# Kernel optimization log

Measured on AMD Instinct MI355X. Metric: run time of the kernel, lower is better.

## Reference

```python
import jax, jax.numpy as jnp
import numpy as np
from jax import lax

B, N, CIN, H, W = 1, 6, 256, 32, 88
COUT = 80
IMG_H, IMG_W = 256, 704
XB = (-51.2, 51.2, 0.8); YB = (-51.2, 51.2, 0.8); ZB = (-5.0, 3.0, 0.8)
NX, NY, NZ = 128, 128, 10
EPS = 1e-5


def _voxel_coords(b0, b1, vs):
    n = int(round((b1 - b0) / vs))
    return jnp.linspace(b0 + 0.5 * vs, b1 - 0.5 * vs, n, dtype=jnp.float32)


def _make_points():
    xs = _voxel_coords(*XB); ys = _voxel_coords(*YB); zs = _voxel_coords(*ZB)
    gx, gy, gz = jnp.meshgrid(xs, ys, zs, indexing='ij')
    return jnp.stack([gx, gy, gz], -1).reshape(-1, 3)  # [M,3], M = NX*NY*NZ


def _conv(x, w, b=None, pad=1):
    y = lax.conv_general_dilated(x, w, (1, 1), [(pad, pad), (pad, pad)],
                                 dimension_numbers=('NCHW', 'OIHW', 'NCHW'))
    if b is not None:
        y = y + b[None, :, None, None]
    return y


def _bn(x, g, b, m, v):
    return (g[None, :, None, None] * (x - m[None, :, None, None])
            * lax.rsqrt(v[None, :, None, None] + EPS) + b[None, :, None, None])


def _bilinear(feat, gx, gy):
    # feat [C,Hf,Wf]; gx,gy [M] in [-1,1]; align_corners=True, zero padding
    C, Hf, Wf = feat.shape
    ix = (gx + 1.0) * 0.5 * (Wf - 1)
    iy = (gy + 1.0) * 0.5 * (Hf - 1)
    ix0 = jnp.floor(ix); iy0 = jnp.floor(iy)
    wx1 = ix - ix0; wy1 = iy - iy0

    def tap(iyf, ixf, wgt):
        valid = (ixf >= 0) & (ixf < Wf) & (iyf >= 0) & (iyf < Hf)
        ii = jnp.clip(ixf, 0, Wf - 1).astype(jnp.int32)
        jj = jnp.clip(iyf, 0, Hf - 1).astype(jnp.int32)
        return feat[:, jj, ii] * (wgt * valid)[None, :]

    return (tap(iy0, ix0, (1 - wy1) * (1 - wx1))
            + tap(iy0, ix0 + 1, (1 - wy1) * wx1)
            + tap(iy0 + 1, ix0, wy1 * (1 - wx1))
            + tap(iy0 + 1, ix0 + 1, wy1 * wx1))


def reference(img, lidar2image, w1, b1, g1, beta1, m1, v1,
              w2, b2, g2, beta2, m2, v2, w3, b3):
    # proj_net: conv3x3+BN+ReLU, conv3x3+BN+ReLU, conv1x1
    x = img.reshape(B * N, CIN, H, W)
    x = jax.nn.relu(_bn(_conv(x, w1, b1), g1, beta1, m1, v1))
    x = jax.nn.relu(_bn(_conv(x, w2, b2), g2, beta2, m2, v2))
    feat = _conv(x, w3, b3, pad=0)  # [B*N, COUT, H, W]

    pts = _make_points()  # [M,3]
    R = lidar2image[:, :, :3, :3].reshape(B * N, 3, 3)
    t = lidar2image[:, :, :3, 3].reshape(B * N, 3, 1)
    proj = jnp.einsum('kij,mj->kim', R, pts) + t  # [BN,3,M]
    dist = proj[:, 2]
    px = proj[:, 0] / dist
    py = proj[:, 1] / dist
    gx = px / IMG_W * 2.0 - 1.0
    gy = py / IMG_H * 2.0 - 1.0

    sampled = jax.vmap(_bilinear)(feat, gx, gy)  # [BN, COUT, M]
    on_img = (px < IMG_W) & (px > 0) & (py < IMG_H) & (py > 0) & (dist > 0.1)
    sampled = jnp.where(on_img[:, None, :], sampled, 0.0)

    vox = sampled.reshape(B, N, COUT, NX, NY, NZ)
    bev = jnp.max(vox, axis=1).mean(axis=-1)  # [B, COUT, NX, NY]
    return bev


def setup_inputs() -> dict:
    key = jax.random.key(0)
    ks = jax.random.split(key, 8)
    img = jax.random.normal(ks[0], (B, N, CIN, H, W), jnp.float32)

    # Plausible lidar->image matrices: 6 cameras in a ring, pinhole intrinsics.
    fx = fy = 280.0; cx = IMG_W / 2.0; cy = IMG_H / 2.0
    K = np.array([[fx, 0.0, cx], [0.0, fy, cy], [0.0, 0.0, 1.0]])
    mats = []
    for k in range(N):
        th = 2.0 * np.pi * k / N
        fwd = np.array([np.cos(th), np.sin(th), 0.0])
        rgt = np.array([np.sin(th), -np.cos(th), 0.0])
        dwn = np.array([0.0, 0.0, -1.0])
        Rm = np.stack([rgt, dwn, fwd], 0)
        c = np.array([0.5 * np.cos(th), 0.5 * np.sin(th), 1.5])
        M4 = np.eye(4)
        M4[:3, :3] = K @ Rm
        M4[:3, 3] = K @ (-Rm @ c)
        mats.append(M4)
    lidar2image = jnp.asarray(np.broadcast_to(np.stack(mats), (B, N, 4, 4)).copy(),
                              jnp.float32)

    def w(k, shape, s=0.02):
        return jax.random.normal(k, shape, jnp.float32) * s

    zc = lambda c: jnp.zeros((c,), jnp.float32)
    oc = lambda c: jnp.ones((c,), jnp.float32)
    return dict(
        img=img, lidar2image=lidar2image,
        w1=w(ks[1], (CIN, CIN, 3, 3)), b1=zc(CIN),
        g1=oc(CIN), beta1=zc(CIN), m1=zc(CIN), v1=oc(CIN),
        w2=w(ks[2], (CIN, CIN, 3, 3)), b2=zc(CIN),
        g2=oc(CIN), beta2=zc(CIN), m2=zc(CIN), v2=oc(CIN),
        w3=w(ks[3], (COUT, CIN, 1, 1)), b3=zc(COUT),
    )
```

## Files before the change

### kernel.cpp

```cpp
#include <hip/hip_runtime.h>
#include <math.h>

#define N_IMG 6
#define CIN   256
#define H_IN  32
#define W_IN  88
#define SP    2816
#define COUTC 80
#define EPSBN 1e-5f

typedef _Float16 half8 __attribute__((ext_vector_type(8)));
typedef float floatx4 __attribute__((ext_vector_type(4)));

__global__ __launch_bounds__(256) void prep_w33(const float* __restrict__ w,
                                                _Float16* __restrict__ wT) {
  int idx = blockIdx.x * 256 + threadIdx.x;
  if (idx >= 9 * CIN * CIN) return;
  int oc  = idx / 2304;
  int r   = idx - oc * 2304;
  int tap = r >> 8;
  int ic  = r & 255;
  wT[idx] = (_Float16)w[(oc * CIN + ic) * 9 + tap];
}

__global__ __launch_bounds__(256) void prep_w11(const float* __restrict__ w,
                                                _Float16* __restrict__ wT) {
  int idx = blockIdx.x * 256 + threadIdx.x;
  if (idx >= CIN * COUTC) return;
  wT[idx] = (_Float16)w[idx];
}

__global__ __launch_bounds__(256) void nchw_to_nhwc(const float* __restrict__ img,
                                                    _Float16* __restrict__ x0) {
  __shared__ float t[64][65];
  const int sp0 = blockIdx.x * 64;
  const int ic0 = blockIdx.y * 64;
  const int im  = blockIdx.z;
  const int tx = threadIdx.x & 63;
  const int ty = threadIdx.x >> 6;
  for (int r = ty; r < 64; r += 4)
    t[r][tx] = img[((size_t)(im * CIN + ic0 + r)) * SP + sp0 + tx];
  __syncthreads();
  for (int r = ty; r < 64; r += 4)
    x0[((size_t)im * SP + sp0 + r) * CIN + ic0 + tx] = (_Float16)t[tx][r];
}

__global__ __launch_bounds__(256) void conv3x3_mfma(
    const _Float16* __restrict__ x, const _Float16* __restrict__ wT,
    const float* __restrict__ bias, const float* __restrict__ gamma,
    const float* __restrict__ beta, const float* __restrict__ bnm,
    const float* __restrict__ bnv, _Float16* __restrict__ out)
{
  __shared__ _Float16 As[128 * 72];
  __shared__ _Float16 Bs[128 * 72];

  const int tid = threadIdx.x;
  const int m0 = blockIdx.x * 128;
  const int n0 = blockIdx.y * 128;
  const int im = blockIdx.z;

  int rr[4], kk4[4], hh[4], ww[4];
  #pragma unroll
  for (int i = 0; i < 4; ++i) {
    const int c = tid + 256 * i;
    rr[i]  = c >> 3;
    kk4[i] = (c & 7) * 8;
    const int m = m0 + rr[i];
    hh[i] = m / 88;
    ww[i] = m - hh[i] * 88;
  }
  const _Float16* xim = x + (size_t)im * SP * CIN;

  const int lane = tid & 63;
  const int wv = tid >> 6;
  const int mw = (wv & 1) * 64;
  const int nw = (wv >> 1) * 64;
  const int fr = lane & 15;
  const int q8 = (lane >> 4) * 8;
  const int q4 = (lane >> 4) * 4;

  floatx4 acc[4][4];
  #pragma unroll
  for (int i = 0; i < 4; ++i)
    #pragma unroll
    for (int j = 0; j < 4; ++j) {
      acc[i][j][0] = 0.f; acc[i][j][1] = 0.f; acc[i][j][2] = 0.f; acc[i][j][3] = 0.f;
    }

  for (int tap = 0; tap < 9; ++tap) {
    const int dy = tap / 3 - 1;
    const int dx = tap - (tap / 3) * 3 - 1;
    bool val[4]; int sp[4];
    #pragma unroll
    for (int i = 0; i < 4; ++i) {
      const int hy = hh[i] + dy, wx = ww[i] + dx;
      val[i] = (hy >= 0) && (hy < H_IN) && (wx >= 0) && (wx < W_IN);
      sp[i] = hy * 88 + wx;
    }

    for (int icc = 0; icc < 256; icc += 64) {
      half8 av[4], bv[4];
      #pragma unroll
      for (int i = 0; i < 4; ++i) {
        half8 z = {};
        av[i] = val[i] ? *(const half8*)(xim + (size_t)sp[i] * CIN + icc + kk4[i]) : z;
        bv[i] = *(const half8*)(wT + (size_t)(n0 + rr[i]) * 2304 + tap * 256 + icc + kk4[i]);
      }
      #pragma unroll
      for (int i = 0; i < 4; ++i) {
        *(half8*)(&As[rr[i] * 72 + kk4[i]]) = av[i];
        *(half8*)(&Bs[rr[i] * 72 + kk4[i]]) = bv[i];
      }
      __syncthreads();

      const _Float16* Ab = &As[(mw + fr) * 72 + q8];
      const _Float16* Bb = &Bs[(nw + fr) * 72 + q8];
      #pragma unroll
      for (int ks = 0; ks < 2; ++ks) {
        half8 af[4], bf[4];
        #pragma unroll
        for (int i = 0; i < 4; ++i) af[i] = *(const half8*)(Ab + i * (16 * 72) + ks * 32);
        #pragma unroll
        for (int j = 0; j < 4; ++j) bf[j] = *(const half8*)(Bb + j * (16 * 72) + ks * 32);
        #pragma unroll
        for (int i = 0; i < 4; ++i)
          #pragma unroll
          for (int j = 0; j < 4; ++j)
            acc[i][j] = __builtin_amdgcn_mfma_f32_16x16x32_f16(af[i], bf[j], acc[i][j], 0, 0, 0);
      }
      __syncthreads();
    }
  }

  #pragma unroll
  for (int j = 0; j < 4; ++j) {
    const int oc = n0 + nw + j * 16 + fr;
    const float sc = gamma[oc] * rsqrtf(bnv[oc] + EPSBN);
    const float sh = (bias[oc] - bnm[oc]) * sc + beta[oc];
    #pragma unroll
    for (int i = 0; i < 4; ++i) {
      const int mbase = m0 + mw + i * 16 + q4;
      #pragma unroll
      for (int r = 0; r < 4; ++r) {
        const float v = fmaxf(fmaf(acc[i][j][r], sc, sh), 0.f);
        out[((size_t)im * SP + mbase + r) * CIN + oc] = (_Float16)v;
      }
    }
  }
}

__global__ __launch_bounds__(256) void conv1x1_mfma(
    const _Float16* __restrict__ x, const _Float16* __restrict__ wT,
    const float* __restrict__ bias, float* __restrict__ feat)
{
  __shared__ _Float16 As[128 * 72];
  __shared__ _Float16 Bs[80 * 72];

  const int tid = threadIdx.x;
  const int m0 = blockIdx.x * 128;

  int rr[4], kk4[4];
  #pragma unroll
  for (int i = 0; i < 4; ++i) {
    const int c = tid + 256 * i;
    rr[i]  = c >> 3;
    kk4[i] = (c & 7) * 8;
  }
  const int rB0 = tid >> 3,         kB0 = (tid & 7) * 8;
  const int rB1 = (tid + 256) >> 3, kB1 = kB0;
  const int rB2 = (tid + 512) >> 3, kB2 = kB0;

  const int lane = tid & 63;
  const int wv = tid >> 6;
  const int mw = wv * 32;
  const int fr = lane & 15;
  const int q8 = (lane >> 4) * 8;
  const int q4 = (lane >> 4) * 4;

  floatx4 acc[2][5];
  #pragma unroll
  for (int i = 0; i < 2; ++i)
    #pragma unroll
    for (int j = 0; j < 5; ++j) {
      acc[i][j][0] = 0.f; acc[i][j][1] = 0.f; acc[i][j][2] = 0.f; acc[i][j][3] = 0.f;
    }

  for (int icc = 0; icc < 256; icc += 64) {
    half8 av[4];
    #pragma unroll
    for (int i = 0; i < 4; ++i)
      av[i] = *(const half8*)(x + (size_t)(m0 + rr[i]) * CIN + icc + kk4[i]);
    half8 b0 = *(const half8*)(wT + (size_t)rB0 * CIN + icc + kB0);
    half8 b1 = *(const half8*)(wT + (size_t)rB1 * CIN + icc + kB1);
    half8 b2 = {};
    if (tid < 128) b2 = *(const half8*)(wT + (size_t)rB2 * CIN + icc + kB2);

    #pragma unroll
    for (int i = 0; i < 4; ++i)
      *(half8*)(&As[rr[i] * 72 + kk4[i]]) = av[i];
    *(half8*)(&Bs[rB0 * 72 + kB0]) = b0;
    *(half8*)(&Bs[rB1 * 72 + kB1]) = b1;
    if (tid < 128) *(half8*)(&Bs[rB2 * 72 + kB2]) = b2;
    __syncthreads();

    const _Float16* Ab = &As[(mw + fr) * 72 + q8];
    const _Float16* Bb = &Bs[fr * 72 + q8];
    #pragma unroll
    for (int ks = 0; ks < 2; ++ks) {
      half8 af[2], bf[5];
      #pragma unroll
      for (int i = 0; i < 2; ++i) af[i] = *(const half8*)(Ab + i * (16 * 72) + ks * 32);
      #pragma unroll
      for (int j = 0; j < 5; ++j) bf[j] = *(const half8*)(Bb + j * (16 * 72) + ks * 32);
      #pragma unroll
      for (int i = 0; i < 2; ++i)
        #pragma unroll
        for (int j = 0; j < 5; ++j)
          acc[i][j] = __builtin_amdgcn_mfma_f32_16x16x32_f16(af[i], bf[j], acc[i][j], 0, 0, 0);
    }
    __syncthreads();
  }

  #pragma unroll
  for (int j = 0; j < 5; ++j) {
    const int oc = j * 16 + fr;
    const float bb = bias[oc];
    #pragma unroll
    for (int i = 0; i < 2; ++i) {
      const int mbase = m0 + mw + i * 16 + q4;
      #pragma unroll
      for (int r = 0; r < 4; ++r)
        feat[(size_t)(mbase + r) * COUTC + oc] = acc[i][j][r] + bb;
    }
  }
}

__global__ __launch_bounds__(320) void bev_sample(
    const float* __restrict__ feat, const float* __restrict__ l2i,
    float* __restrict__ tmp)
{
  __shared__ int4   eo[240];
  __shared__ float4 ew[240];
  const int tid = threadIdx.x;
  const int cellBase = blockIdx.x * 4;

  if (tid < 240) {
    const int cell = tid / 60;
    const int e = tid - cell * 60;
    const int n = e / 10;
    const int z = e - n * 10;
    const int cid = cellBase + cell;
    const int gix = cid >> 7;
    const int giy = cid & 127;
    const float X = (float)(-50.8 + (double)gix * (101.6 / 127.0));
    const float Y = (float)(-50.8 + (double)giy * (101.6 / 127.0));
    const float Z = (float)(-4.6 + (double)z * (7.2 / 9.0));
    const float* M = l2i + n * 16;
    const float pw = M[0] * X + M[1] * Y + M[2] * Z + M[3];
    const float ph = M[4] * X + M[5] * Y + M[6] * Z + M[7];
    const float d  = M[8] * X + M[9] * Y + M[10] * Z + M[11];
    const float px = pw / d;
    const float py = ph / d;
    const bool on_img = (px < 704.f) && (px > 0.f) && (py < 256.f) && (py > 0.f) && (d > 0.1f);
    const float gx = px / 704.f * 2.f - 1.f;
    const float gy = py / 256.f * 2.f - 1.f;
    const float ixf = (gx + 1.f) * 0.5f * 87.f;
    const float iyf = (gy + 1.f) * 0.5f * 31.f;
    const float ix0 = floorf(ixf);
    const float iy0 = floorf(iyf);
    const float wx1 = ixf - ix0;
    const float wy1 = iyf - iy0;
    const float ix1 = ix0 + 1.f, iy1 = iy0 + 1.f;
    float w00 = (1.f - wy1) * (1.f - wx1);
    float w01 = (1.f - wy1) * wx1;
    float w10 = wy1 * (1.f - wx1);
    float w11 = wy1 * wx1;
    const bool vx0 = (ix0 >= 0.f) && (ix0 < 88.f);
    const bool vx1 = (ix1 >= 0.f) && (ix1 < 88.f);
    const bool vy0 = (iy0 >= 0.f) && (iy0 < 32.f);
    const bool vy1 = (iy1 >= 0.f) && (iy1 < 32.f);
    if (!(on_img && vy0 && vx0)) w00 = 0.f;
    if (!(on_img && vy0 && vx1)) w01 = 0.f;
    if (!(on_img && vy1 && vx0)) w10 = 0.f;
    if (!(on_img && vy1 && vx1)) w11 = 0.f;
    const int i0 = (int)fminf(fmaxf(ix0, 0.f), 87.f);
    const int i1 = (int)fminf(fmaxf(ix1, 0.f), 87.f);
    const int j0 = (int)fminf(fmaxf(iy0, 0.f), 31.f);
    const int j1 = (int)fminf(fmaxf(iy1, 0.f), 31.f);
    const int base = n * SP;
    eo[tid] = make_int4((base + j0 * 88 + i0) * COUTC,
                        (base + j0 * 88 + i1) * COUTC,
                        (base + j1 * 88 + i0) * COUTC,
                        (base + j1 * 88 + i1) * COUTC);
    ew[tid] = make_float4(w00, w01, w10, w11);
  }
  __syncthreads();

  const int c = tid % 80;
  const int cell = tid / 80;
  const int ebase = cell * 60;
  float acc = 0.f;
  for (int z = 0; z < 10; ++z) {
    float mx = -INFINITY;
    #pragma unroll
    for (int n = 0; n < 6; ++n) {
      const int4   o = eo[ebase + n * 10 + z];
      const float4 w = ew[ebase + n * 10 + z];
      float v = w.x * feat[o.x + c];
      v = fmaf(w.y, feat[o.y + c], v);
      v = fmaf(w.z, feat[o.z + c], v);
      v = fmaf(w.w, feat[o.w + c], v);
      mx = fmaxf(mx, v);
    }
    acc += mx;
  }
  tmp[(size_t)(cellBase + cell) * COUTC + c] = acc / 10.f;
}

__global__ __launch_bounds__(256) void bev_transpose(const float* __restrict__ tmp,
                                                     float* __restrict__ out)
{
  __shared__ float tile[32][33];
  const int mBase = blockIdx.x * 32;
  const int cBase = blockIdx.y * 32;
  const int tx = threadIdx.x & 31;
  const int ty = threadIdx.x >> 5;
  for (int i = ty; i < 32; i += 8) {
    const int cc = cBase + tx;
    tile[i][tx] = (cc < COUTC) ? tmp[(size_t)(mBase + i) * COUTC + cc] : 0.f;
  }
  __syncthreads();
  for (int i = ty; i < 32; i += 8) {
    const int cc = cBase + i;
    if (cc < COUTC) out[(size_t)cc * 16384 + mBase + tx] = tile[tx][i];
  }
}

extern "C" void kernel_launch(void* const* d_in, const int* in_sizes, int n_in,
                              void* d_out, int out_size, void* d_ws, size_t ws_size,
                              hipStream_t stream)
{
  const float* img = (const float*)d_in[0];
  const float* l2i = (const float*)d_in[1];
  const float* w1  = (const float*)d_in[2];
  const float* b1  = (const float*)d_in[3];
  const float* g1  = (const float*)d_in[4];
  const float* be1 = (const float*)d_in[5];
  const float* m1  = (const float*)d_in[6];
  const float* v1  = (const float*)d_in[7];
  const float* w2  = (const float*)d_in[8];
  const float* b2  = (const float*)d_in[9];
  const float* g2  = (const float*)d_in[10];
  const float* be2 = (const float*)d_in[11];
  const float* m2  = (const float*)d_in[12];
  const float* v2  = (const float*)d_in[13];
  const float* w3  = (const float*)d_in[14];
  const float* b3  = (const float*)d_in[15];

  char* ws = (char*)d_ws;
  _Float16* wT1h = (_Float16*)ws;                    ws += 9 * CIN * CIN * 2;
  _Float16* wT2h = (_Float16*)ws;                    ws += 9 * CIN * CIN * 2;
  _Float16* wT3h = (_Float16*)ws;                    ws += CIN * COUTC * 2;
  _Float16* x0   = (_Float16*)ws;                    ws += (size_t)N_IMG * SP * CIN * 2;
  _Float16* x1h  = (_Float16*)ws;                    ws += (size_t)N_IMG * SP * CIN * 2;
  _Float16* x2h  = (_Float16*)ws;                    ws += (size_t)N_IMG * SP * CIN * 2;
  float*    feat = (float*)ws;                       ws += (size_t)N_IMG * SP * COUTC * 4;
  float*    tmp  = (float*)ws;
  float*    outp = (float*)d_out;

  prep_w33<<<2304, 256, 0, stream>>>(w1, wT1h);
  prep_w33<<<2304, 256, 0, stream>>>(w2, wT2h);
  prep_w11<<<80, 256, 0, stream>>>(w3, wT3h);
  nchw_to_nhwc<<<dim3(44, 4, 6), 256, 0, stream>>>(img, x0);

  conv3x3_mfma<<<dim3(22, 2, 6), 256, 0, stream>>>(x0, wT1h, b1, g1, be1, m1, v1, x1h);
  conv3x3_mfma<<<dim3(22, 2, 6), 256, 0, stream>>>(x1h, wT2h, b2, g2, be2, m2, v2, x2h);
  conv1x1_mfma<<<132, 256, 0, stream>>>(x2h, wT3h, b3, feat);

  bev_sample<<<4096, 320, 0, stream>>>(feat, l2i, tmp);
  bev_transpose<<<dim3(512, 3), 256, 0, stream>>>(tmp, outp);
}
```

Measured before the change: 260.5 us.

## Pad conv inputs, stream activations via global_load_lds, fp16 feat, rebatch BEV sampling

Convolution inputs are stored in a zero-padded 34x90 NHWC layout so the 3x3 conv can drop per-tap boundary checks. Activation tiles are loaded straight into an XOR-swizzled LDS buffer with global_load_lds, while weights are read directly from global memory into registers. The output-channel tile shrinks to 64, which doubles the grid. The 1x1 conv output becomes fp16, bev_sample processes 8 cells per block with two channels per thread, and the weight prep kernel transposes through shared memory. The trade-offs are two extra memsets, more global weight traffic per block, and lower precision in the sampled features.

```diff
diff --git a/kernel.cpp b/kernel.cpp
--- a/kernel.cpp
+++ b/kernel.cpp
@@ -6,21 +6,29 @@
 #define H_IN  32
 #define W_IN  88
 #define SP    2816
+#define HH    34
+#define WW    90
+#define SPH   3060
 #define COUTC 80
 #define EPSBN 1e-5f
 
 typedef _Float16 half8 __attribute__((ext_vector_type(8)));
+typedef _Float16 half2v __attribute__((ext_vector_type(2)));
 typedef float floatx4 __attribute__((ext_vector_type(4)));
 
 __global__ __launch_bounds__(256) void prep_w33(const float* __restrict__ w,
                                                 _Float16* __restrict__ wT) {
-  int idx = blockIdx.x * 256 + threadIdx.x;
-  if (idx >= 9 * CIN * CIN) return;
-  int oc  = idx / 2304;
-  int r   = idx - oc * 2304;
-  int tap = r >> 8;
-  int ic  = r & 255;
-  wT[idx] = (_Float16)w[(oc * CIN + ic) * 9 + tap];
+  __shared__ float s[2304];
+  const int oc = blockIdx.x;
+  const int tid = threadIdx.x;
+  const float* wo = w + (size_t)oc * 2304;
+  for (int i = tid; i < 2304; i += 256) s[i] = wo[i];
+  __syncthreads();
+  for (int i = tid; i < 2304; i += 256) {
+    const int tap = i >> 8;
+    const int ic  = i & 255;
+    wT[(size_t)oc * 2304 + i] = (_Float16)s[ic * 9 + tap];
+  }
 }
 
 __global__ __launch_bounds__(256) void prep_w11(const float* __restrict__ w,
@@ -41,109 +49,117 @@
   for (int r = ty; r < 64; r += 4)
     t[r][tx] = img[((size_t)(im * CIN + ic0 + r)) * SP + sp0 + tx];
   __syncthreads();
-  for (int r = ty; r < 64; r += 4)
-    x0[((size_t)im * SP + sp0 + r) * CIN + ic0 + tx] = (_Float16)t[tx][r];
+  for (int r = ty; r < 64; r += 4) {
+    const int sp = sp0 + r;
+    const int h = sp / 88;
+    const int w = sp - h * 88;
+    x0[((size_t)im * SPH + h * WW + w + WW + 1) * CIN + ic0 + tx] = (_Float16)t[tx][r];
+  }
 }
 
 __global__ __launch_bounds__(256) void conv3x3_mfma(
     const _Float16* __restrict__ x, const _Float16* __restrict__ wT,
     const float* __restrict__ bias, const float* __restrict__ gamma,
     const float* __restrict__ beta, const float* __restrict__ bnm,
-    const float* __restrict__ bnv, _Float16* __restrict__ out)
+    const float* __restrict__ bnv, _Float16* __restrict__ out,
+    int OW, int OB, int imStride)
 {
-  __shared__ _Float16 As[128 * 72];
-  __shared__ _Float16 Bs[128 * 72];
+  __shared__ _Float16 As[128 * 64];
 
   const int tid = threadIdx.x;
   const int m0 = blockIdx.x * 128;
-  const int n0 = blockIdx.y * 128;
+  const int n0 = blockIdx.y * 64;
   const int im = blockIdx.z;
-
-  int rr[4], kk4[4], hh[4], ww[4];
+  const _Float16* xim = x + (size_t)im * SPH * CIN;
+
+  int sBase[4];
   #pragma unroll
   for (int i = 0; i < 4; ++i) {
-    const int c = tid + 256 * i;
-    rr[i]  = c >> 3;
-    kk4[i] = (c & 7) * 8;
-    const int m = m0 + rr[i];
-    hh[i] = m / 88;
-    ww[i] = m - hh[i] * 88;
-  }
-  const _Float16* xim = x + (size_t)im * SP * CIN;
-
+    const int c = tid + i * 256;
+    const int row = c >> 3;
+    const int m = m0 + row;
+    const int h = m / 88;
+    const int w = m - h * 88;
+    sBase[i] = ((h + 1) * WW + (w + 1)) * CIN + (((c & 7) ^ (row & 7)) * 8);
+  }
+
+  const int wv   = tid >> 6;
   const int lane = tid & 63;
-  const int wv = tid >> 6;
-  const int mw = (wv & 1) * 64;
-  const int nw = (wv >> 1) * 64;
-  const int fr = lane & 15;
-  const int q8 = (lane >> 4) * 8;
-  const int q4 = (lane >> 4) * 4;
-
-  floatx4 acc[4][4];
+  const int fr   = lane & 15;
+  const int q    = lane >> 4;
+  const int q8   = q * 8;
+  const int q4   = q * 4;
+  const int mw   = (wv & 1) * 64;
+  const int nw   = (wv >> 1) * 32;
+  const int fr7  = fr & 7;
+
+  const _Float16* wrow0 = wT + (size_t)(n0 + nw + fr) * 2304 + q8;
+  const _Float16* wrow1 = wT + (size_t)(n0 + nw + 16 + fr) * 2304 + q8;
+
+  floatx4 acc[4][2];
   #pragma unroll
   for (int i = 0; i < 4; ++i)
     #pragma unroll
-    for (int j = 0; j < 4; ++j) {
+    for (int j = 0; j < 2; ++j) {
       acc[i][j][0] = 0.f; acc[i][j][1] = 0.f; acc[i][j][2] = 0.f; acc[i][j][3] = 0.f;
     }
 
   for (int tap = 0; tap < 9; ++tap) {
     const int dy = tap / 3 - 1;
     const int dx = tap - (tap / 3) * 3 - 1;
-    bool val[4]; int sp[4];
-    #pragma unroll
-    for (int i = 0; i < 4; ++i) {
-      const int hy = hh[i] + dy, wx = ww[i] + dx;
-      val[i] = (hy >= 0) && (hy < H_IN) && (wx >= 0) && (wx < W_IN);
-      sp[i] = hy * 88 + wx;
-    }
-
+    const int dtap = (dy * WW + dx) * CIN;
+
+    #pragma unroll
     for (int icc = 0; icc < 256; icc += 64) {
-      half8 av[4], bv[4];
+      const int woff = tap * 256 + icc;
+      half8 bf00 = *(const half8*)(wrow0 + woff);
+      half8 bf01 = *(const half8*)(wrow0 + woff + 32);
+      half8 bf10 = *(const half8*)(wrow1 + woff);
+      half8 bf11 = *(const half8*)(wrow1 + woff + 32);
       #pragma unroll
       for (int i = 0; i < 4; ++i) {
-        half8 z = {};
-        av[i] = val[i] ? *(const half8*)(xim + (size_t)sp[i] * CIN + icc + kk4[i]) : z;
-        bv[i] = *(const half8*)(wT + (size_t)(n0 + rr[i]) * 2304 + tap * 256 + icc + kk4[i]);
-      }
-      #pragma unroll
-      for (int i = 0; i < 4; ++i) {
-        *(half8*)(&As[rr[i] * 72 + kk4[i]]) = av[i];
-        *(half8*)(&Bs[rr[i] * 72 + kk4[i]]) = bv[i];
+        __builtin_amdgcn_global_load_lds(
+            (const __attribute__((address_space(1))) void*)(xim + sBase[i] + dtap + icc),
+            (__attribute__((address_space(3))) void*)(&As[(wv * 64 + i * 256) * 8]),
+            16, 0, 0);
       }
       __syncthreads();
 
-      const _Float16* Ab = &As[(mw + fr) * 72 + q8];
-      const _Float16* Bb = &Bs[(nw + fr) * 72 + q8];
       #pragma unroll
       for (int ks = 0; ks < 2; ++ks) {
-        half8 af[4], bf[4];
+        half8 af[4];
         #pragma unroll
-        for (int i = 0; i < 4; ++i) af[i] = *(const half8*)(Ab + i * (16 * 72) + ks * 32);
+        for (int i = 0; i < 4; ++i) {
+          const int row = mw + i * 16 + fr;
+          const int phys = (ks * 4 + q) ^ fr7;
+          af[i] = *(const half8*)(&As[row * 64 + phys * 8]);
+        }
+        const half8 b0 = ks ? bf01 : bf00;
+        const half8 b1 = ks ? bf11 : bf10;
         #pragma unroll
-        for (int j = 0; j < 4; ++j) bf[j] = *(const half8*)(Bb + j * (16 * 72) + ks * 32);
-        #pragma unroll
-        for (int i = 0; i < 4; ++i)
-          #pragma unroll
-          for (int j = 0; j < 4; ++j)
-            acc[i][j] = __builtin_amdgcn_mfma_f32_16x16x32_f16(af[i], bf[j], acc[i][j], 0, 0, 0);
+        for (int i = 0; i < 4; ++i) {
+          acc[i][0] = __builtin_amdgcn_mfma_f32_16x16x32_f16(af[i], b0, acc[i][0], 0, 0, 0);
+          acc[i][1] = __builtin_amdgcn_mfma_f32_16x16x32_f16(af[i], b1, acc[i][1], 0, 0, 0);
+        }
       }
       __syncthreads();
     }
   }
 
   #pragma unroll
-  for (int j = 0; j < 4; ++j) {
+  for (int j = 0; j < 2; ++j) {
     const int oc = n0 + nw + j * 16 + fr;
     const float sc = gamma[oc] * rsqrtf(bnv[oc] + EPSBN);
     const float sh = (bias[oc] - bnm[oc]) * sc + beta[oc];
     #pragma unroll
     for (int i = 0; i < 4; ++i) {
-      const int mbase = m0 + mw + i * 16 + q4;
       #pragma unroll
       for (int r = 0; r < 4; ++r) {
+        const int m = m0 + mw + i * 16 + q4 + r;
+        const int h = m / 88;
+        const int w = m - h * 88;
         const float v = fmaxf(fmaf(acc[i][j][r], sc, sh), 0.f);
-        out[((size_t)im * SP + mbase + r) * CIN + oc] = (_Float16)v;
+        out[((size_t)im * imStride + h * OW + w + OB) * CIN + oc] = (_Float16)v;
       }
     }
   }
@@ -151,7 +167,7 @@
 
 __global__ __launch_bounds__(256) void conv1x1_mfma(
     const _Float16* __restrict__ x, const _Float16* __restrict__ wT,
-    const float* __restrict__ bias, float* __restrict__ feat)
+    const float* __restrict__ bias, _Float16* __restrict__ feat)
 {
   __shared__ _Float16 As[128 * 72];
   __shared__ _Float16 Bs[80 * 72];
@@ -207,16 +223,16 @@
     const _Float16* Bb = &Bs[fr * 72 + q8];
     #pragma unroll
     for (int ks = 0; ks < 2; ++ks) {
-      half8 af[2], bf[5];
+      half8 af[2], bfv[5];
       #pragma unroll
       for (int i = 0; i < 2; ++i) af[i] = *(const half8*)(Ab + i * (16 * 72) + ks * 32);
       #pragma unroll
-      for (int j = 0; j < 5; ++j) bf[j] = *(const half8*)(Bb + j * (16 * 72) + ks * 32);
+      for (int j = 0; j < 5; ++j) bfv[j] = *(const half8*)(Bb + j * (16 * 72) + ks * 32);
       #pragma unroll
       for (int i = 0; i < 2; ++i)
         #pragma unroll
         for (int j = 0; j < 5; ++j)
-          acc[i][j] = __builtin_amdgcn_mfma_f32_16x16x32_f16(af[i], bf[j], acc[i][j], 0, 0, 0);
+          acc[i][j] = __builtin_amdgcn_mfma_f32_16x16x32_f16(af[i], bfv[j], acc[i][j], 0, 0, 0);
     }
     __syncthreads();
   }
@@ -230,25 +246,25 @@
       const int mbase = m0 + mw + i * 16 + q4;
       #pragma unroll
       for (int r = 0; r < 4; ++r)
-        feat[(size_t)(mbase + r) * COUTC + oc] = acc[i][j][r] + bb;
+        feat[(size_t)(mbase + r) * COUTC + oc] = (_Float16)(acc[i][j][r] + bb);
     }
   }
 }
 
 __global__ __launch_bounds__(320) void bev_sample(
-    const float* __restrict__ feat, const float* __restrict__ l2i,
+    const _Float16* __restrict__ feat, const float* __restrict__ l2i,
     float* __restrict__ tmp)
 {
-  __shared__ int4   eo[240];
-  __shared__ float4 ew[240];
+  __shared__ int4   eo[480];
+  __shared__ float4 ew[480];
   const int tid = threadIdx.x;
-  const int cellBase = blockIdx.x * 4;
-
-  if (tid < 240) {
-    const int cell = tid / 60;
-    const int e = tid - cell * 60;
-    const int n = e / 10;
-    const int z = e - n * 10;
+  const int cellBase = blockIdx.x * 8;
+
+  for (int e = tid; e < 480; e += 320) {
+    const int cell = e / 60;
+    const int idx = e - cell * 60;
+    const int n = idx / 10;
+    const int z = idx - n * 10;
     const int cid = cellBase + cell;
     const int gix = cid >> 7;
     const int giy = cid & 127;
@@ -288,33 +304,42 @@
     const int j0 = (int)fminf(fmaxf(iy0, 0.f), 31.f);
     const int j1 = (int)fminf(fmaxf(iy1, 0.f), 31.f);
     const int base = n * SP;
-    eo[tid] = make_int4((base + j0 * 88 + i0) * COUTC,
-                        (base + j0 * 88 + i1) * COUTC,
-                        (base + j1 * 88 + i0) * COUTC,
-                        (base + j1 * 88 + i1) * COUTC);
-    ew[tid] = make_float4(w00, w01, w10, w11);
+    eo[e] = make_int4((base + j0 * 88 + i0) * COUTC,
+                      (base + j0 * 88 + i1) * COUTC,
+                      (base + j1 * 88 + i0) * COUTC,
+                      (base + j1 * 88 + i1) * COUTC);
+    ew[e] = make_float4(w00, w01, w10, w11);
   }
   __syncthreads();
 
-  const int c = tid % 80;
-  const int cell = tid / 80;
+  const int c2 = (tid % 40) * 2;
+  const int cell = tid / 40;
   const int ebase = cell * 60;
-  float acc = 0.f;
+  float a0 = 0.f, a1 = 0.f;
   for (int z = 0; z < 10; ++z) {
-    float mx = -INFINITY;
+    float mx0 = -INFINITY, mx1 = -INFINITY;
     #pragma unroll
     for (int n = 0; n < 6; ++n) {
       const int4   o = eo[ebase + n * 10 + z];
       const float4 w = ew[ebase + n * 10 + z];
-      float v = w.x * feat[o.x + c];
-      v = fmaf(w.y, feat[o.y + c], v);
-      v = fmaf(w.z, feat[o.z + c], v);
-      v = fmaf(w.w, feat[o.w + c], v);
-      mx = fmaxf(mx, v);
-    }
-    acc += mx;
-  }
-  tmp[(size_t)(cellBase + cell) * COUTC + c] = acc / 10.f;
+      const half2v p00 = *(const half2v*)(feat + o.x + c2);
+      const half2v p01 = *(const half2v*)(feat + o.y + c2);
+      const half2v p10 = *(const half2v*)(feat + o.z + c2);
+      const half2v p11 = *(const half2v*)(feat + o.w + c2);
+      float v0 = w.x * (float)p00[0];
+      float v1 = w.x * (float)p00[1];
+      v0 = fmaf(w.y, (float)p01[0], v0);  v1 = fmaf(w.y, (float)p01[1], v1);
+      v0 = fmaf(w.z, (float)p10[0], v0);  v1 = fmaf(w.z, (float)p10[1], v1);
+      v0 = fmaf(w.w, (float)p11[0], v0);  v1 = fmaf(w.w, (float)p11[1], v1);
+      mx0 = fmaxf(mx0, v0);
+      mx1 = fmaxf(mx1, v1);
+    }
+    a0 += mx0;
+    a1 += mx1;
+  }
+  const int cid = cellBase + cell;
+  float2 res = make_float2(a0 * 0.1f, a1 * 0.1f);
+  *(float2*)(&tmp[(size_t)cid * COUTC + c2]) = res;
 }
 
 __global__ __launch_bounds__(256) void bev_transpose(const float* __restrict__ tmp,
@@ -358,25 +383,30 @@
   const float* b3  = (const float*)d_in[15];
 
   char* ws = (char*)d_ws;
-  _Float16* wT1h = (_Float16*)ws;                    ws += 9 * CIN * CIN * 2;
-  _Float16* wT2h = (_Float16*)ws;                    ws += 9 * CIN * CIN * 2;
-  _Float16* wT3h = (_Float16*)ws;                    ws += CIN * COUTC * 2;
-  _Float16* x0   = (_Float16*)ws;                    ws += (size_t)N_IMG * SP * CIN * 2;
-  _Float16* x1h  = (_Float16*)ws;                    ws += (size_t)N_IMG * SP * CIN * 2;
-  _Float16* x2h  = (_Float16*)ws;                    ws += (size_t)N_IMG * SP * CIN * 2;
-  float*    feat = (float*)ws;                       ws += (size_t)N_IMG * SP * COUTC * 4;
+  _Float16* wT1h = (_Float16*)ws;  ws += (size_t)9 * CIN * CIN * 2;
+  _Float16* wT2h = (_Float16*)ws;  ws += (size_t)9 * CIN * CIN * 2;
+  _Float16* wT3h = (_Float16*)ws;  ws += (size_t)CIN * COUTC * 2;
+  _Float16* x0   = (_Float16*)ws;  ws += (size_t)N_IMG * SPH * CIN * 2;
+  _Float16* x1h  = (_Float16*)ws;  ws += (size_t)N_IMG * SPH * CIN * 2;
+  _Float16* x2h  = (_Float16*)ws;  ws += (size_t)N_IMG * SP * CIN * 2;
+  _Float16* feat = (_Float16*)ws;  ws += (size_t)N_IMG * SP * COUTC * 2;
   float*    tmp  = (float*)ws;
   float*    outp = (float*)d_out;
 
-  prep_w33<<<2304, 256, 0, stream>>>(w1, wT1h);
-  prep_w33<<<2304, 256, 0, stream>>>(w2, wT2h);
+  hipMemsetAsync(x0,  0, (size_t)N_IMG * SPH * CIN * 2, stream);
+  hipMemsetAsync(x1h, 0, (size_t)N_IMG * SPH * CIN * 2, stream);
+
+  prep_w33<<<256, 256, 0, stream>>>(w1, wT1h);
+  prep_w33<<<256, 256, 0, stream>>>(w2, wT2h);
   prep_w11<<<80, 256, 0, stream>>>(w3, wT3h);
   nchw_to_nhwc<<<dim3(44, 4, 6), 256, 0, stream>>>(img, x0);
 
-  conv3x3_mfma<<<dim3(22, 2, 6), 256, 0, stream>>>(x0, wT1h, b1, g1, be1, m1, v1, x1h);
-  conv3x3_mfma<<<dim3(22, 2, 6), 256, 0, stream>>>(x1h, wT2h, b2, g2, be2, m2, v2, x2h);
+  conv3x3_mfma<<<dim3(22, 4, 6), 256, 0, stream>>>(x0, wT1h, b1, g1, be1, m1, v1,
+                                                   x1h, WW, WW + 1, SPH);
+  conv3x3_mfma<<<dim3(22, 4, 6), 256, 0, stream>>>(x1h, wT2h, b2, g2, be2, m2, v2,
+                                                   x2h, 88, 0, SP);
   conv1x1_mfma<<<132, 256, 0, stream>>>(x2h, wT3h, b3, feat);
 
-  bev_sample<<<4096, 320, 0, stream>>>(feat, l2i, tmp);
+  bev_sample<<<2048, 320, 0, stream>>>(feat, l2i, tmp);
   bev_transpose<<<dim3(512, 3), 256, 0, stream>>>(tmp, outp);
 }
```

Result: slower. 305.9 us (+17.4%).
